# Kernel optimization log

Hardware: AMD Instinct MI355X
Metric: run time of the kernel (lower is better)

## Reference

```python
import jax, jax.numpy as jnp
import numpy as np
from jax import lax

BN_EPS = 1e-5
B, C_IN, HW = 512, 3, 128  # crop batch, channels, crop size
C1, C2 = 32, 64
DIST_THRESHOLD = 0.55


def setup_inputs() -> dict:
    key = jax.random.key(0)
    ks = jax.random.split(key, 13)
    return {
        "crops": jax.random.normal(ks[0], (B, C_IN, HW, HW), jnp.float32),
        "w1": jax.random.normal(ks[1], (C1, C_IN, 3, 3), jnp.float32) * 0.1,
        "b1": jax.random.normal(ks[2], (C1,), jnp.float32) * 0.1,
        "g1": jax.random.uniform(ks[3], (C1,), jnp.float32),
        "be1": jax.random.normal(ks[4], (C1,), jnp.float32) * 0.1,
        "m1": jax.random.normal(ks[5], (C1,), jnp.float32) * 0.1,
        "v1": jax.random.uniform(ks[6], (C1,), jnp.float32),
        "w2": jax.random.normal(ks[7], (C2, C1, 3, 3), jnp.float32) * 0.05,
        "b2": jax.random.normal(ks[8], (C2,), jnp.float32) * 0.1,
        "g2": jax.random.uniform(ks[9], (C2,), jnp.float32),
        "be2": jax.random.normal(ks[10], (C2,), jnp.float32) * 0.1,
        "m2": jax.random.normal(ks[11], (C2,), jnp.float32) * 0.1,
        "v2": jax.random.uniform(ks[12], (C2,), jnp.float32),
    }


def _conv(x, w, b, stride):
    y = lax.conv_general_dilated(
        x, w, window_strides=(stride, stride), padding=((1, 1), (1, 1)),
        dimension_numbers=("NCHW", "OIHW", "NCHW"))
    return y + b[None, :, None, None]


def _bn(x, gamma, beta, mean, var):
    inv = gamma * lax.rsqrt(var + BN_EPS)
    return x * inv[None, :, None, None] + (beta - mean * inv)[None, :, None, None]


def _maxpool2(x):
    return lax.reduce_window(x, -jnp.inf, lax.max, (1, 1, 2, 2), (1, 1, 2, 2), "VALID")


def reference(crops, w1, b1, g1, be1, m1, v1, w2, b2, g2, be2, m2, v2):
    # layer1: Conv(3->32, s1, p1) + BN + ReLU + MaxPool2  -> [B, 32, 64, 64]
    h = _maxpool2(jax.nn.relu(_bn(_conv(crops, w1, b1, 1), g1, be1, m1, v1)))
    # layer2: Conv(32->64, s2, p1) + BN + Sigmoid + MaxPool2 -> [B, 64, 16, 16]
    feat = _maxpool2(jax.nn.sigmoid(_bn(_conv(h, w2, b2, 2), g2, be2, m2, v2)))
    # per-crop distribution score thresholded as in uniqueDistribution/MLE
    scores = feat.mean(axis=(1, 2, 3))            # [B]
    detected = scores >= DIST_THRESHOLD           # [B] bool
    return feat, scores, detected
```

## Files before the change

### kernel.cpp

```cpp
#include <hip/hip_runtime.h>
#include <math.h>

#define BN_EPS 1e-5f
#define HW_ 128

typedef unsigned short u16_t;
typedef unsigned int u32_t;

typedef __bf16 bf16x8 __attribute__((ext_vector_type(8)));
typedef __bf16 bf16v2 __attribute__((ext_vector_type(2)));
typedef float f32x4 __attribute__((ext_vector_type(4)));
typedef float f32x16 __attribute__((ext_vector_type(16)));
typedef u32_t u32x4 __attribute__((ext_vector_type(4)));
typedef u32_t u32x2 __attribute__((ext_vector_type(2)));
typedef u32x4 u32x4_ma __attribute__((may_alias));
typedef u32x2 u32x2_ma __attribute__((may_alias));
typedef f32x4 f32x4_ma __attribute__((may_alias));

static __device__ __forceinline__ u16_t f2bf(float f) {
    union { __bf16 v; u16_t u; } x;
    x.v = (__bf16)f;
    return x.u;
}
static __device__ __forceinline__ u32_t packbf(float a, float b) {
    union { bf16v2 v; u32_t u; } x;
    bf16v2 p;
    p[0] = (__bf16)a;
    p[1] = (__bf16)b;
    x.v = p;
    return x.u;
}
static __device__ __forceinline__ bf16x8 ld_frag16(const u16_t* p) {
    union { u32x4 u; bf16x8 f; } x;
    x.u = *(const u32x4_ma*)p;
    return x.f;
}
static __device__ __forceinline__ bf16x8 ld_frag32(const u32_t* p) {
    union { u32x4 u; bf16x8 f; } x;
    x.u = *(const u32x4_ma*)p;
    return x.f;
}
static __device__ __forceinline__ bf16x8 asbf(u32x4 u) {
    union { u32x4 u; bf16x8 f; } x;
    x.u = u;
    return x.f;
}

#define WSUM_OFF 0
#define W2R_OFF  512
#define WF_OFF   9728
#define PT_OFF   10496
#define BN1_OFF  13056
#define BN2_OFF  13120
#define WS_TOTAL 13248

#define CI_U32   (36 * 74)

__global__ __launch_bounds__(512) void prep_kernel(
    const float* __restrict__ w1, const float* __restrict__ b1,
    const float* __restrict__ g1, const float* __restrict__ be1,
    const float* __restrict__ m1, const float* __restrict__ v1,
    const float* __restrict__ w2, const float* __restrict__ b2,
    const float* __restrict__ g2, const float* __restrict__ be2,
    const float* __restrict__ m2, const float* __restrict__ v2,
    u32_t* __restrict__ ws)
{
    const int gtid = blockIdx.x * 512 + threadIdx.x;

    if (gtid < 512) ws[WSUM_OFF + gtid] = 0u;

    for (int idx = gtid; idx < 9216; idx += 8192) {
        int H   = idx / 4608;
        int rem = idx - H * 4608;
        int tap = rem >> 9;
        int r2  = rem & 511;
        int ocl = r2 >> 4;
        int icp = r2 & 15;
        const float* wp = w2 + (H * 32 + ocl) * 288 + tap;
        ws[W2R_OFF + idx] = packbf(wp[(2 * icp) * 9], wp[(2 * icp + 1) * 9]);
    }
    if (gtid < 192) {
        int s = gtid >> 6, lane = gtid & 63;
        int n32 = lane & 31, h = lane >> 5;
        u32x4 f;
        #pragma unroll
        for (int jp = 0; jp < 4; ++jp) {
            int j0 = 2 * jp, j1 = 2 * jp + 1;
            int kx0 = 2 * h + (j0 >> 2), ch0 = j0 & 3;
            int kx1 = 2 * h + (j1 >> 2), ch1 = j1 & 3;
            float va = (kx0 < 3 && ch0 < 3) ? w1[n32 * 27 + ch0 * 9 + s * 3 + kx0] : 0.f;
            float vb = (kx1 < 3 && ch1 < 3) ? w1[n32 * 27 + ch1 * 9 + s * 3 + kx1] : 0.f;
            f[jp] = packbf(va, vb);
        }
        ((u32x4_ma*)(ws + WF_OFF))[gtid] = f;
    }
    if (gtid < 2560) {
        int tt = gtid >> 6, lane = gtid & 63;
        int n32 = lane & 31, h = lane >> 5;
        int gA = n32 >> 2, sub = n32 & 3;
        int pA = tt * 8 + gA;
        int gy = (pA * 241) >> 12; gy = min(gy, 16);
        int gx = min(pA - gy * 17, 16); gx = max(gx, 0);
        int cy = 2 * gy + (sub >> 1), cx = 2 * gx + (sub & 1);
        ws[PT_OFF + gtid] = (u32_t)((cy * 37 + cx + 2 * h) * 2);
    }
    if (gtid >= 1024 && gtid < 1056) {
        int ch = gtid - 1024;
        float inv = g1[ch] * rsqrtf(v1[ch] + BN_EPS);
        float sh  = b1[ch] * inv + be1[ch] - m1[ch] * inv;
        ws[BN1_OFF + 2 * ch]     = __float_as_uint(inv);
        ws[BN1_OFF + 2 * ch + 1] = __float_as_uint(sh);
    }
    if (gtid >= 2048 && gtid < 2112) {
        int ch = gtid - 2048;
        float inv = g2[ch] * rsqrtf(v2[ch] + BN_EPS);
        float sh  = b2[ch] * inv + be2[ch] - m2[ch] * inv;
        ws[BN2_OFF + 2 * ch]     = __float_as_uint(inv);
        ws[BN2_OFF + 2 * ch + 1] = __float_as_uint(sh);
    }
}

__global__ __launch_bounds__(512, 8) void fused_cnn_kernel(
    const float* __restrict__ crops, const u32_t* __restrict__ tab,
    float* __restrict__ out, float* __restrict__ wsum)
{
    __shared__ __align__(16) u32_t uniS[CI_U32];
    __shared__ __align__(16) u16_t hS[289 * 32];
    __shared__ float redS[8];

    const int tid  = threadIdx.x;
    const int wave = tid >> 6;
    const int lane = tid & 63;
    const int quad = lane >> 4;
    const int r    = lane & 15;
    const int n32  = lane & 31;
    const int halfk = lane >> 5;

    const int blk = ((blockIdx.x & 7) << 10) | (blockIdx.x >> 3);
    const int img = blk >> 4;
    const int t   = blk & 15;
    const int fy0 = (t >> 2) * 4;
    const int fx0 = (t & 3) * 4;
    const int crop_y0 = 8 * fy0 - 3;
    const int crop_x0 = 8 * fx0 - 3;
    const bool interior = (fy0 != 0) && (fx0 != 0);

    const float* cbase = crops + (size_t)img * (3 * HW_ * HW_);
    const int x0a = crop_x0 - 1;
    if (tid < 360) {
        int row = (tid * 6554) >> 16;
        int vec = tid - row * 10;
        int gr  = crop_y0 + row;
        int col0 = x0a + 4 * vec;
        f32x4 c0 = {0.f,0.f,0.f,0.f}, c1 = {0.f,0.f,0.f,0.f}, c2 = {0.f,0.f,0.f,0.f};
        if ((unsigned)gr < 128u) {
            const float* rp = cbase + gr * HW_;
            if (col0 >= 0 && col0 <= 124) {
                c0 = *(const f32x4_ma*)(rp + col0);
                c1 = *(const f32x4_ma*)(rp + HW_ * HW_ + col0);
                c2 = *(const f32x4_ma*)(rp + 2 * HW_ * HW_ + col0);
            } else {
                #pragma unroll
                for (int j = 0; j < 4; ++j) {
                    int gc = col0 + j;
                    if ((unsigned)gc < 128u) {
                        c0[j] = rp[gc];
                        c1[j] = rp[HW_ * HW_ + gc];
                        c2[j] = rp[2 * HW_ * HW_ + gc];
                    }
                }
            }
        }
        const int ccb = 4 * vec - 1;
        u32_t* up = uniS + (row * 37 + ccb) * 2;
        #pragma unroll
        for (int j = 0; j < 4; ++j) {
            if ((unsigned)(ccb + j) < 37u) {
                u32x2 w;
                w[0] = packbf(c0[j], c1[j]);
                w[1] = packbf(c2[j], 0.f);
                *(u32x2_ma*)(up + 2 * j) = w;
            }
        }
    }

    u32x4 wf[3];
    const u32x4_ma* wft = (const u32x4_ma*)(tab + WF_OFF);
    #pragma unroll
    for (int s = 0; s < 3; ++s) wf[s] = wft[s * 64 + lane];
    u32_t pofs[5];
    #pragma unroll
    for (int i = 0; i < 5; ++i) pofs[i] = tab[PT_OFF + (wave + 8 * i) * 64 + lane];
    const float inv1 = __uint_as_float(tab[BN1_OFF + 2 * n32]);
    const float sh1  = __uint_as_float(tab[BN1_OFF + 2 * n32 + 1]);
    __syncthreads();

    const int hsub = n32 & 7;
    const int hchk = n32 >> 3;
    const int pbase = wave * 8 + halfk;

    int hqi[4];
    #pragma unroll
    for (int q = 0; q < 4; ++q)
        hqi[q] = wave * 256 + halfk * 32 + hsub + q * 64 + ((hchk ^ q) << 3);

    const f32x16 z16 = {0.f,0.f,0.f,0.f,0.f,0.f,0.f,0.f,
                        0.f,0.f,0.f,0.f,0.f,0.f,0.f,0.f};

    auto conv_trip = [&](int ii) -> f32x16 {
        const u32_t* bp = uniS + pofs[ii];
        u32x2 l0a = *(const u32x2_ma*)(bp);
        u32x2 l0b = *(const u32x2_ma*)(bp + 2);
        u32x2 l1a = *(const u32x2_ma*)(bp + 74);
        u32x2 l1b = *(const u32x2_ma*)(bp + 76);
        u32x2 l2a = *(const u32x2_ma*)(bp + 148);
        u32x2 l2b = *(const u32x2_ma*)(bp + 150);
        u32x4 a0; a0[0] = l0a[0]; a0[1] = l0a[1]; a0[2] = l0b[0]; a0[3] = l0b[1];
        u32x4 a1; a1[0] = l1a[0]; a1[1] = l1a[1]; a1[2] = l1b[0]; a1[3] = l1b[1];
        u32x4 a2; a2[0] = l2a[0]; a2[1] = l2a[1]; a2[2] = l2b[0]; a2[3] = l2b[1];
        f32x16 acc = __builtin_amdgcn_mfma_f32_32x32x16_bf16(asbf(a0), asbf(wf[0]), z16, 0, 0, 0);
        acc = __builtin_amdgcn_mfma_f32_32x32x16_bf16(asbf(a1), asbf(wf[1]), acc, 0, 0, 0);
        acc = __builtin_amdgcn_mfma_f32_32x32x16_bf16(asbf(a2), asbf(wf[2]), acc, 0, 0, 0);
        return acc;
    };

    auto pool_val = [&](int ii, int q, const f32x16& acc) -> float {
        float m4 = fmaxf(fmaxf(fmaxf(acc[4 * q], acc[4 * q + 1]), acc[4 * q + 2]),
                         acc[4 * q + 3]);
        float val = fmaxf(fmaf(m4, inv1, sh1), 0.f);
        if (!interior) {
            int pD  = pbase + ii * 64 + 2 * q;
            int gyD = (pD * 241) >> 12;
            int gxD = pD - gyD * 17;
            int y2 = 4 * fy0 - 1 + gyD, x2 = 4 * fx0 - 1 + gxD;
            if (y2 < 0 || y2 > 63 || x2 < 0 || x2 > 63) val = 0.f;
        }
        return val;
    };

    #pragma unroll
    for (int i = 0; i < 4; ++i) {
        f32x16 acc = conv_trip(i);
        #pragma unroll
        for (int q = 0; q < 4; ++q)
            hS[hqi[q] + i * 2048] = f2bf(pool_val(i, q, acc));
    }
    if (wave < 4) {
        f32x16 acc = conv_trip(4);
        #pragma unroll
        for (int q = 0; q < 4; ++q)
            hS[hqi[q] + 4 * 2048] = f2bf(pool_val(4, q, acc));
    } else if (wave == 4) {
        f32x16 acc = conv_trip(4);
        float val = pool_val(4, 0, acc);
        if (halfk == 0) hS[hqi[0] + 4 * 2048] = f2bf(val);
    }
    __syncthreads();

    float* outp = out + (size_t)img * 16384;
    const f32x4 zero4 = {0.f, 0.f, 0.f, 0.f};
    const int mt  = wave & 1;
    const int nt0 = wave >> 1;
    const int cy2 = 2 * nt0 + ((r >> 1) & 1);
    const int cx2 = 2 * (r >> 2) + (r & 1);
    const int fy  = fy0 + nt0;
    const int p0  = 34 * cy2 + 2 * cx2;

    const int oc0 = mt * 16 + r;
    const u32_t* wz0 = tab + W2R_OFF + oc0 * 16 + quad * 4;
    const u32_t* wz1 = wz0 + 4608;
    const float s2_0  = __uint_as_float(tab[BN2_OFF + 2 * oc0]);
    const float sh2_0 = __uint_as_float(tab[BN2_OFF + 2 * oc0 + 1]);
    const float s2_1  = __uint_as_float(tab[BN2_OFF + 64 + 2 * oc0]);
    const float sh2_1 = __uint_as_float(tab[BN2_OFF + 64 + 2 * oc0 + 1]);

    auto ld_ah = [&](int p) -> bf16x8 {
        return ld_frag16(&hS[p * 32 + (((quad ^ (p >> 1)) & 3) << 3)]);
    };

    f32x4 acc0 = zero4, acc1 = zero4;
    bf16x8 w0a = ld_frag32(wz0);
    bf16x8 w1a = ld_frag32(wz1);
    bf16x8 w0b = ld_frag32(wz0 + 512);
    bf16x8 w1b = ld_frag32(wz1 + 512);
    bf16x8 ahn = ld_ah(p0);
    #pragma unroll
    for (int s = 0; s < 9; ++s) {
        bf16x8 ah = ahn;
        if (s < 8) {
            const int ns = s + 1;
            const int nky = ns / 3, nkx = ns - 3 * nky;
            ahn = ld_ah(p0 + nky * 17 + nkx);
        }
        bf16x8 cw0 = w0a, cw1 = w1a;
        w0a = w0b; w1a = w1b;
        if (s < 7) {
            w0b = ld_frag32(wz0 + (s + 2) * 512);
            w1b = ld_frag32(wz1 + (s + 2) * 512);
        }
        acc0 = __builtin_amdgcn_mfma_f32_16x16x32_bf16(ah, cw0, acc0, 0, 0, 0);
        acc1 = __builtin_amdgcn_mfma_f32_16x16x32_bf16(ah, cw1, acc1, 0, 0, 0);
    }

    float m40 = fmaxf(fmaxf(fmaxf(acc0[0], acc0[1]), acc0[2]), acc0[3]);
    float z0  = fmaf(m40, s2_0, sh2_0);
    float sig0 = 1.f / (1.f + __expf(-z0));
    outp[oc0 * 256 + fy * 16 + fx0 + quad] = sig0;
    float m41 = fmaxf(fmaxf(fmaxf(acc1[0], acc1[1]), acc1[2]), acc1[3]);
    float z1  = fmaf(m41, s2_1, sh2_1);
    float sig1 = 1.f / (1.f + __expf(-z1));
    outp[(32 + oc0) * 256 + fy * 16 + fx0 + quad] = sig1;
    float ssum = sig0 + sig1;

    #pragma unroll
    for (int off = 32; off > 0; off >>= 1)
        ssum += __shfl_xor(ssum, off);
    if (lane == 0) redS[wave] = ssum;
    __syncthreads();
    if (tid == 0) {
        float bs = 0.f;
        #pragma unroll
        for (int w = 0; w < 8; ++w) bs += redS[w];
        atomicAdd(&wsum[img], bs);
    }
}

__global__ void finalize_kernel(const float* __restrict__ ws,
                                float* __restrict__ scores,
                                float* __restrict__ detected) {
    int i = threadIdx.x;
    float mean = ws[i] * (1.f / 16384.f);
    scores[i] = mean;
    detected[i] = (mean >= 0.55f) ? 1.f : 0.f;
}

extern "C" void kernel_launch(void* const* d_in, const int* in_sizes, int n_in,
                              void* d_out, int out_size, void* d_ws, size_t ws_size,
                              hipStream_t stream) {
    (void)in_sizes; (void)n_in; (void)out_size; (void)ws_size;
    const float* crops = (const float*)d_in[0];
    const float* w1  = (const float*)d_in[1];
    const float* b1  = (const float*)d_in[2];
    const float* g1  = (const float*)d_in[3];
    const float* be1 = (const float*)d_in[4];
    const float* m1  = (const float*)d_in[5];
    const float* v1  = (const float*)d_in[6];
    const float* w2  = (const float*)d_in[7];
    const float* b2  = (const float*)d_in[8];
    const float* g2  = (const float*)d_in[9];
    const float* be2 = (const float*)d_in[10];
    const float* m2  = (const float*)d_in[11];
    const float* v2  = (const float*)d_in[12];
    float* out = (float*)d_out;
    u32_t* ws  = (u32_t*)d_ws;

    prep_kernel<<<16, 512, 0, stream>>>(
        w1, b1, g1, be1, m1, v1, w2, b2, g2, be2, m2, v2, ws);
    fused_cnn_kernel<<<8192, 512, 0, stream>>>(
        crops, ws, out, (float*)ws);
    finalize_kernel<<<1, 512, 0, stream>>>(
        (const float*)ws, out + 8388608, out + 8388608 + 512);
}
```

Baseline: 257.3 us.

## Fold finalize into last block, pad hS pitch, raise MFMA priority

Drops the separate finalize kernel. Each block now increments a done counter after its atomic sum, and the last block to finish writes scores and detected flags, which saves a launch. The layer-1 output buffer in shared memory is padded from a pitch of 32 to 40 bf16 per pixel to reduce LDS bank conflicts, at the cost of more LDS per block. s_setprio is raised around the MFMA sections to favour matrix issue across waves. The larger LDS footprint could reduce occupancy, and the last-block pattern adds an extra atomic and a barrier to every block.

```diff
diff --git a/kernel.cpp b/kernel.cpp
--- a/kernel.cpp
+++ b/kernel.cpp
@@ -52,9 +52,11 @@
 #define PT_OFF   10496
 #define BN1_OFF  13056
 #define BN2_OFF  13120
-#define WS_TOTAL 13248
+#define DONE_OFF 13248
+#define WS_TOTAL 13249
 
 #define CI_U32   (36 * 74)
+#define HS_PITCH 40
 
 __global__ __launch_bounds__(512) void prep_kernel(
     const float* __restrict__ w1, const float* __restrict__ b1,
@@ -68,6 +70,7 @@
     const int gtid = blockIdx.x * 512 + threadIdx.x;
 
     if (gtid < 512) ws[WSUM_OFF + gtid] = 0u;
+    if (gtid == 512) ws[DONE_OFF] = 0u;
 
     for (int idx = gtid; idx < 9216; idx += 8192) {
         int H   = idx / 4608;
@@ -125,7 +128,7 @@
     float* __restrict__ out, float* __restrict__ wsum)
 {
     __shared__ __align__(16) u32_t uniS[CI_U32];
-    __shared__ __align__(16) u16_t hS[289 * 32];
+    __shared__ __align__(16) u16_t hS[289 * HS_PITCH];
     __shared__ float redS[8];
 
     const int tid  = threadIdx.x;
@@ -202,7 +205,7 @@
     int hqi[4];
     #pragma unroll
     for (int q = 0; q < 4; ++q)
-        hqi[q] = wave * 256 + halfk * 32 + hsub + q * 64 + ((hchk ^ q) << 3);
+        hqi[q] = (wave * 8 + halfk + 2 * q) * HS_PITCH + ((hchk ^ q) << 3) + hsub;
 
     const f32x16 z16 = {0.f,0.f,0.f,0.f,0.f,0.f,0.f,0.f,
                         0.f,0.f,0.f,0.f,0.f,0.f,0.f,0.f};
@@ -218,9 +221,11 @@
         u32x4 a0; a0[0] = l0a[0]; a0[1] = l0a[1]; a0[2] = l0b[0]; a0[3] = l0b[1];
         u32x4 a1; a1[0] = l1a[0]; a1[1] = l1a[1]; a1[2] = l1b[0]; a1[3] = l1b[1];
         u32x4 a2; a2[0] = l2a[0]; a2[1] = l2a[1]; a2[2] = l2b[0]; a2[3] = l2b[1];
+        __builtin_amdgcn_s_setprio(1);
         f32x16 acc = __builtin_amdgcn_mfma_f32_32x32x16_bf16(asbf(a0), asbf(wf[0]), z16, 0, 0, 0);
         acc = __builtin_amdgcn_mfma_f32_32x32x16_bf16(asbf(a1), asbf(wf[1]), acc, 0, 0, 0);
         acc = __builtin_amdgcn_mfma_f32_32x32x16_bf16(asbf(a2), asbf(wf[2]), acc, 0, 0, 0);
+        __builtin_amdgcn_s_setprio(0);
         return acc;
     };
 
@@ -243,17 +248,17 @@
         f32x16 acc = conv_trip(i);
         #pragma unroll
         for (int q = 0; q < 4; ++q)
-            hS[hqi[q] + i * 2048] = f2bf(pool_val(i, q, acc));
+            hS[hqi[q] + i * (64 * HS_PITCH)] = f2bf(pool_val(i, q, acc));
     }
     if (wave < 4) {
         f32x16 acc = conv_trip(4);
         #pragma unroll
         for (int q = 0; q < 4; ++q)
-            hS[hqi[q] + 4 * 2048] = f2bf(pool_val(4, q, acc));
+            hS[hqi[q] + 4 * (64 * HS_PITCH)] = f2bf(pool_val(4, q, acc));
     } else if (wave == 4) {
         f32x16 acc = conv_trip(4);
         float val = pool_val(4, 0, acc);
-        if (halfk == 0) hS[hqi[0] + 4 * 2048] = f2bf(val);
+        if (halfk == 0) hS[hqi[0] + 4 * (64 * HS_PITCH)] = f2bf(val);
     }
     __syncthreads();
 
@@ -275,7 +280,7 @@
     const float sh2_1 = __uint_as_float(tab[BN2_OFF + 64 + 2 * oc0 + 1]);
 
     auto ld_ah = [&](int p) -> bf16x8 {
-        return ld_frag16(&hS[p * 32 + (((quad ^ (p >> 1)) & 3) << 3)]);
+        return ld_frag16(&hS[p * HS_PITCH + (((quad ^ (p >> 1)) & 3) << 3)]);
     };
 
     f32x4 acc0 = zero4, acc1 = zero4;
@@ -284,6 +289,7 @@
     bf16x8 w0b = ld_frag32(wz0 + 512);
     bf16x8 w1b = ld_frag32(wz1 + 512);
     bf16x8 ahn = ld_ah(p0);
+    __builtin_amdgcn_s_setprio(1);
     #pragma unroll
     for (int s = 0; s < 9; ++s) {
         bf16x8 ah = ahn;
@@ -301,6 +307,7 @@
         acc0 = __builtin_amdgcn_mfma_f32_16x16x32_bf16(ah, cw0, acc0, 0, 0, 0);
         acc1 = __builtin_amdgcn_mfma_f32_16x16x32_bf16(ah, cw1, acc1, 0, 0, 0);
     }
+    __builtin_amdgcn_s_setprio(0);
 
     float m40 = fmaxf(fmaxf(fmaxf(acc0[0], acc0[1]), acc0[2]), acc0[3]);
     float z0  = fmaf(m40, s2_0, sh2_0);
@@ -322,16 +329,18 @@
         #pragma unroll
         for (int w = 0; w < 8; ++w) bs += redS[w];
         atomicAdd(&wsum[img], bs);
-    }
-}
-
-__global__ void finalize_kernel(const float* __restrict__ ws,
-                                float* __restrict__ scores,
-                                float* __restrict__ detected) {
-    int i = threadIdx.x;
-    float mean = ws[i] * (1.f / 16384.f);
-    scores[i] = mean;
-    detected[i] = (mean >= 0.55f) ? 1.f : 0.f;
+        __threadfence();
+        u32_t old = atomicAdd((u32_t*)wsum + DONE_OFF, 1u);
+        redS[0] = (old == 8191u) ? 1.f : 0.f;
+    }
+    __syncthreads();
+    if (redS[0] != 0.f) {
+        __threadfence();
+        float s = atomicAdd(&wsum[tid], 0.0f);
+        float mean = s * (1.f / 16384.f);
+        out[8388608 + tid] = mean;
+        out[8388608 + 512 + tid] = (mean >= 0.55f) ? 1.f : 0.f;
+    }
 }
 
 extern "C" void kernel_launch(void* const* d_in, const int* in_sizes, int n_in,
@@ -358,6 +367,4 @@
         w1, b1, g1, be1, m1, v1, w2, b2, g2, be2, m2, v2, ws);
     fused_cnn_kernel<<<8192, 512, 0, stream>>>(
         crops, ws, out, (float*)ws);
-    finalize_kernel<<<1, 512, 0, stream>>>(
-        (const float*)ws, out + 8388608, out + 8388608 + 512);
-}
+}
```

Measured after the change: 627.9 us. 144% more time.
